# Optimization experiments

Measured on AMD Instinct MI355X. Metric: run time of the kernel, lower is better.

The kernel has to match this reference:

```python
import jax, jax.numpy as jnp
import numpy as np
from jax import lax

# SSD300/COCO geometry
B, P, C = 16, 8732, 81
V_CENTER, V_SIZE = 0.1, 0.2        # box coder variances
SCORE_THRESH = 0.05
NMS_THRESH = 0.45
DETS_PER_IMG = 100
PRE_NMS_TOPK = 1000                # fixed-size candidate set for jit-compatible NMS
MIN_SIZE = 0.01                    # remove_small_boxes threshold


def setup_inputs() -> dict:
    key = jax.random.key(0)
    k1, k2, k3, k4, k5 = jax.random.split(key, 5)
    # scale logits so a realistic fraction of softmax scores clears SCORE_THRESH
    pred_logits = jax.random.normal(k1, (B, P, C), jnp.float32) * 2.0
    pred_boxes = jax.random.normal(k2, (B, P, 4), jnp.float32) * 0.5
    # priors in (cx, cy, w, h), normalized coords, positive sizes
    cxcy = jax.random.uniform(k3, (P, 2), jnp.float32, 0.05, 0.95)
    wh = jax.random.uniform(k4, (P, 2), jnp.float32, 0.02, 0.4)
    priors = jnp.concatenate([cxcy, wh], axis=-1)
    target_sizes = jax.random.randint(k5, (B, 2), 480, 1333)  # (h, w) per image
    return {"pred_logits": pred_logits, "pred_boxes": pred_boxes,
            "priors": priors, "target_sizes": target_sizes}


def _decode(rel, priors):
    # SSD box coder: rel = (dx, dy, dw, dh), priors = (cx, cy, w, h) -> xyxy
    cxcy = priors[:, :2] + rel[:, :2] * V_CENTER * priors[:, 2:]
    wh = priors[:, 2:] * jnp.exp(rel[:, 2:] * V_SIZE)
    return jnp.concatenate([cxcy - 0.5 * wh, cxcy + 0.5 * wh], axis=-1)


def _pairwise_iou(b):
    # b: [K, 4] xyxy
    area = (b[:, 2] - b[:, 0]) * (b[:, 3] - b[:, 1])
    lt = jnp.maximum(b[:, None, :2], b[None, :, :2])
    rb = jnp.minimum(b[:, None, 2:], b[None, :, 2:])
    whi = jnp.clip(rb - lt, 0.0)
    inter = whi[..., 0] * whi[..., 1]
    return inter / (area[:, None] + area[None, :] - inter + 1e-9)


def _per_image(logits, rel, priors, size_hw):
    nc1 = C - 1  # foreground classes
    # decode and scale to pixel coords: target_size.flip(0).repeat(2) = [w, h, w, h]
    size_hw = size_hw.astype(jnp.float32)
    whwh = jnp.concatenate([size_hw[::-1], size_hw[::-1]])
    boxes = _decode(rel, priors) * whwh                     # [P, 4]
    scores = jax.nn.softmax(logits, axis=-1)[:, 1:]          # [P, C-1], drop background
    # score threshold + remove_small_boxes, fused as a mask (jit-safe)
    size_ok = ((boxes[:, 2] - boxes[:, 0]) >= MIN_SIZE) & \
              ((boxes[:, 3] - boxes[:, 1]) >= MIN_SIZE)      # [P]
    valid = (scores > SCORE_THRESH) & size_ok[:, None]       # [P, C-1]
    s_flat = jnp.where(valid, scores, -1.0).reshape(-1)      # [P*(C-1)]
    vals, idx = lax.top_k(s_flat, PRE_NMS_TOPK)
    prior_idx = idx // nc1
    labels_k = idx % nc1 + 1                                 # class ids in [1, C)
    boxes_k = boxes[prior_idx]                               # [K, 4]
    vmask = vals > 0.0                                       # real candidates
    # batched_nms via per-class coordinate offset
    max_coord = jnp.max(jnp.where(vmask[:, None], boxes_k, 0.0))
    offs_boxes = boxes_k + (labels_k.astype(jnp.float32) * (max_coord + 1.0))[:, None]
    iou = _pairwise_iou(offs_boxes)                          # [K, K]
    cols = jnp.arange(PRE_NMS_TOPK)

    def body(i, keep):
        suppress = (iou[i] > NMS_THRESH) & keep[i] & (cols > i)
        return keep & ~suppress

    keep = lax.fori_loop(0, PRE_NMS_TOPK, body, vmask)
    kept_scores = jnp.where(keep, vals, -1.0)
    fvals, fidx = lax.top_k(kept_scores, DETS_PER_IMG)
    fvalid = fvals > 0.0
    out_boxes = jnp.where(fvalid[:, None], boxes_k[fidx], 0.0)
    out_scores = jnp.where(fvalid, fvals, 0.0)
    out_labels = jnp.where(fvalid, labels_k[fidx], -1)
    return out_boxes, out_scores, out_labels


def reference(pred_logits, pred_boxes, priors, target_sizes):
    boxes, scores, labels = jax.vmap(_per_image, in_axes=(0, 0, None, 0))(
        pred_logits, pred_boxes, priors, target_sizes)
    # padded, fixed-size equivalent of the per-image list of dicts
    return boxes, scores, labels
```

## Files before the change

### kernel.cpp

```cpp
#include <hip/hip_runtime.h>
#include <math.h>

#pragma clang fp contract(off)

#define NIMG 16
#define NP   8732
#define NCLS 81
#define NFG  80
#define KTOP 1000
#define KPAD 1024
#define DETS 100
#define CAPMAX 166912
#define BASEBITS 0x3D000000u
#define CNT_STRIDE 64
#define TILEB 137
#define NB 640

#define OFF_BOXES  0u
#define OFF_CNT    2235392u
#define OFF_GHIST  2239488u
#define OFF_CSCORE 2280448u
#define OFF_CLABEL 2345984u
#define OFF_CBOX   2411520u
#define OFF_COFFS  2673664u
#define OFF_CAREA  2935808u
#define OFF_VALIDW 3001344u
#define OFF_MASK   3003392u
#define OFF_CAND   5100544u
#define MEMSET_LEN 45056u

typedef unsigned long long u64;
typedef unsigned int u32;

#define AS_GLOBAL __attribute__((address_space(1)))
#define AS_LOCAL  __attribute__((address_space(3)))

__global__ __launch_bounds__(256, 6) void k_decode(
    const float* __restrict__ logits, const float* __restrict__ rel,
    const float* __restrict__ priors, const int* __restrict__ tsz,
    float* __restrict__ boxes_out, u64* __restrict__ cand,
    u32* __restrict__ cnt, u32* __restrict__ ghist, int cap)
{
#pragma clang fp contract(off)
    __shared__ __align__(16) float lx[64 * NCLS];
    __shared__ float pmx[4 * 64];
    __shared__ float psm[4 * 64];
    __shared__ u32 sok[64];
    __shared__ u32 wtt[4];
    __shared__ u32 sbase;
    __shared__ u32 lhist[NB];
    int b  = blockIdx.x / TILEB;
    int g  = blockIdx.x - b * TILEB;
    int p0 = g * 64;
    int t  = threadIdx.x;
    int lane = t & 63;
    int q = t >> 6;
    int npri = NP - p0; if (npri > 64) npri = 64;
    int words = npri * NCLS;

    const u32* s32 = (const u32*)(logits + ((size_t)b * NP + p0) * NCLS);
    u32* lxw = (u32*)lx;
    int full = words >> 8;
    for (int k = q; k < full; k += 4)
        __builtin_amdgcn_global_load_lds(
            (AS_GLOBAL const u32*)(s32 + (k << 8) + (lane << 2)),
            (AS_LOCAL u32*)(lxw + (k << 8)), 16, 0, 0);
    int base = full << 8;
    int c4 = (words - base) >> 6;
    for (int k = q; k < c4; k += 4)
        __builtin_amdgcn_global_load_lds(
            (AS_GLOBAL const u32*)(s32 + base + (k << 6) + lane),
            (AS_LOCAL u32*)(lxw + base + (k << 6)), 4, 0, 0);
    int base2 = base + (c4 << 6);
    if (q == 0 && lane < words - base2) lxw[base2 + lane] = s32[base2 + lane];

    for (int i = t; i < NB; i += 256) lhist[i] = 0;

    int p = p0 + lane;
    bool active = p < NP;

    if (q == 0) {
        u32 ok = 0;
        if (active) {
            float4 pr = ((const float4*)priors)[p];
            float4 rl = ((const float4*)rel)[(size_t)b * NP + p];
            float W = (float)tsz[b * 2 + 1], H = (float)tsz[b * 2 + 0];
            float cx = pr.x + (rl.x * 0.1f) * pr.z;
            float cy = pr.y + (rl.y * 0.1f) * pr.w;
            float w_ = pr.z * expf(rl.z * 0.2f);
            float h_ = pr.w * expf(rl.w * 0.2f);
            float4 bx;
            bx.x = (cx - 0.5f * w_) * W; bx.y = (cy - 0.5f * h_) * H;
            bx.z = (cx + 0.5f * w_) * W; bx.w = (cy + 0.5f * h_) * H;
            ((float4*)boxes_out)[(size_t)b * NP + p] = bx;
            ok = ((bx.z - bx.x) >= 0.01f) && ((bx.w - bx.y) >= 0.01f);
        }
        sok[lane] = ok;
    }
    __syncthreads();

    int tb = lane * NCLS;
    int nk = (q == 0) ? 21 : 20;
    float x[21];
    #pragma unroll
    for (int k = 0; k < 21; ++k) {
        int c = q + 4 * k;
        x[k] = (k < nk) ? lx[tb + c] : -3.4e38f;
    }
    float pm = -3.4e38f;
    #pragma unroll
    for (int k = 0; k < 21; ++k) if (k < nk) pm = fmaxf(pm, x[k]);
    pmx[q * 64 + lane] = pm;
    __syncthreads();
    float m = fmaxf(fmaxf(pmx[lane], pmx[64 + lane]),
                    fmaxf(pmx[128 + lane], pmx[192 + lane]));

    float ps = 0.f;
    #pragma unroll
    for (int k = 0; k < 21; ++k) {
        if (k < nk) { x[k] = expf(x[k] - m); ps += x[k]; }
    }
    psm[q * 64 + lane] = ps;
    __syncthreads();
    float s = (psm[lane] + psm[64 + lane]) + (psm[128 + lane] + psm[192 + lane]);

    float hi = 0.05000075f * s;
    float lo = 0.04999925f * s;
    u32 pass = 0, band = 0;
    u32 sizeok = sok[lane];
    if (active && sizeok) {
        #pragma unroll
        for (int k = 0; k < 21; ++k) {
            int c = q + 4 * k;
            if (k < nk && c >= 1) {
                bool pa = x[k] > hi;
                bool bd = (!pa) && (x[k] > lo);
                pass |= ((u32)pa) << k;
                band |= ((u32)bd) << k;
            }
        }
    }
    while (band) {
        int k = __builtin_ctz(band); band &= band - 1;
        int c = q + 4 * k;
        float e = expf(lx[tb + c] - m);
        if (e / s > 0.05f) pass |= 1u << k;
    }
    int cnt_t = __popc(pass);

    int pre = cnt_t;
    #pragma unroll
    for (int d = 1; d < 64; d <<= 1) {
        int o = __shfl_up(pre, d);
        if (lane >= d) pre += o;
    }
    if (lane == 63) wtt[q] = (u32)pre;
    __syncthreads();
    u32 before = 0;
    for (int w = 0; w < 4; ++w) if (w < q) before += wtt[w];
    if (t == 0) {
        u32 tot = wtt[0] + wtt[1] + wtt[2] + wtt[3];
        sbase = tot ? atomicAdd(cnt + b * CNT_STRIDE, tot) : 0u;
    }
    __syncthreads();
    u32 pos = sbase + before + (u32)(pre - cnt_t);

    u64* cb = cand + (size_t)b * cap;
    u32 flatneg = 0xFFFFFFFFu - (u32)p * NFG;
    while (pass) {
        int k = __builtin_ctz(pass); pass &= pass - 1;
        int c = q + 4 * k;
        float e = expf(lx[tb + c] - m);
        float d = e / s;
        if ((int)pos < cap) {
            u32 sb = __float_as_uint(d);
            cb[pos] = ((u64)sb << 32) | (u64)(flatneg - (u32)(c - 1));
            u32 bin = (sb - BASEBITS) >> 16; if (bin > NB - 1) bin = NB - 1;
            atomicAdd(&lhist[bin], 1u);
        }
        ++pos;
    }
    __syncthreads();
    u32* gh = ghist + b * NB;
    for (int i = t; i < NB; i += 256) {
        u32 v = lhist[i];
        if (v) atomicAdd(gh + i, v);
    }
}

__device__ __forceinline__ void suffix_find(
    u32* hist, u32* wt, u32 K, int tid,
    volatile int* outI, volatile u32* outNext)
{
    int lane = tid & 63, w = tid >> 6;
    u32 v[8]; u32 tot = 0;
    #pragma unroll
    for (int k = 0; k < 8; ++k) { v[k] = hist[tid * 8 + k]; tot += v[k]; }
    u32 ws = tot;
    #pragma unroll
    for (int d = 1; d < 64; d <<= 1) {
        u32 o = __shfl_down(ws, d);
        if (lane + d < 64) ws += o;
    }
    if (lane == 0) wt[w] = ws;
    __syncthreads();
    u32 tail = 0;
    for (int w2 = w + 1; w2 < 16; ++w2) tail += wt[w2];
    u32 after = (ws - tot) + tail;
    u32 sufk[9];
    sufk[8] = after;
    #pragma unroll
    for (int k = 7; k >= 0; --k) sufk[k] = v[k] + sufk[k + 1];
    #pragma unroll
    for (int k = 0; k < 8; ++k) {
        if (sufk[k] >= K && sufk[k + 1] < K) {
            *outI = tid * 8 + k;
            *outNext = sufk[k + 1];
        }
    }
    __syncthreads();
}

__global__ __launch_bounds__(1024) void k_select(
    const u64* __restrict__ cand, const u32* __restrict__ cnt,
    const u32* __restrict__ ghist, const float* __restrict__ boxes,
    float* __restrict__ cscore, int* __restrict__ clabel,
    float4* __restrict__ cbox, float4* __restrict__ coffs,
    float* __restrict__ carea, u64* __restrict__ validw, int cap)
{
#pragma clang fp contract(off)
    __shared__ u32 h[NB];
    __shared__ u32 fh[8192];
    __shared__ u32 wt[16];
    __shared__ u64 buf[2048];
    __shared__ float red16[16];
    __shared__ int sh_c, sh_i2;
    __shared__ u32 sh_S, sh_next, sh_d, sh_m;
    int b = blockIdx.x, t = threadIdx.x, lane = t & 63;
    u32 n = min(cnt[b * CNT_STRIDE], (u32)cap);
    const u64* cb = cand + (size_t)b * cap;

    for (int i = t; i < NB; i += 1024) h[i] = ghist[b * NB + i];
    if (t == 0) { sh_c = -2; sh_i2 = -2; sh_S = 0; sh_next = 0; sh_m = 0; }
    __syncthreads();
    if (t < 64) {
        u32 v[10]; u32 tot = 0;
        #pragma unroll
        for (int k = 0; k < 10; ++k) { v[k] = h[t * 10 + k]; tot += v[k]; }
        u32 ws = tot;
        #pragma unroll
        for (int d = 1; d < 64; d <<= 1) {
            u32 o = (u32)__shfl_down((int)ws, d);
            if (t + d < 64) ws += o;
        }
        u32 suf[11];
        suf[10] = ws - tot;
        #pragma unroll
        for (int k = 9; k >= 0; --k) suf[k] = v[k] + suf[k + 1];
        #pragma unroll
        for (int k = 0; k < 10; ++k) {
            if (suf[k] >= (u32)KTOP && suf[k + 1] < (u32)KTOP) {
                sh_c = t * 10 + k; sh_S = suf[k]; sh_next = suf[k + 1];
            }
        }
    }
    __syncthreads();
    int c = sh_c;
    u32 T = 0;
    if (c >= 0) {
        u32 Tc = BASEBITS + ((u32)c << 16);
        if (sh_S <= 2048u) {
            T = Tc;
        } else {
            u32 nhi = sh_next;
            for (int i = t; i < 8192; i += 1024) fh[i] = 0;
            __syncthreads();
            for (u32 i = (u32)t; i < n; i += 1024) {
                u32 sb = (u32)(cb[i] >> 32);
                if ((sb & 0xFFFF0000u) == Tc)
                    atomicAdd(&fh[(sb >> 3) & 0x1FFFu], 1u);
            }
            __syncthreads();
            suffix_find(fh, wt, (u32)KTOP - nhi, t, &sh_i2, &sh_d);
            T = (sh_i2 >= 0) ? (Tc + ((u32)sh_i2 << 3)) : Tc;
        }
    }
    for (u32 bs0 = 0; bs0 < n; bs0 += 4096) {
        u32 i0 = bs0 + (u32)t;
        u64 k0 = 0, k1 = 0, k2 = 0, k3 = 0;
        bool q0 = i0 < n, q1 = i0 + 1024 < n, q2 = i0 + 2048 < n, q3 = i0 + 3072 < n;
        if (q0) k0 = cb[i0];
        if (q1) k1 = cb[i0 + 1024];
        if (q2) k2 = cb[i0 + 2048];
        if (q3) k3 = cb[i0 + 3072];
        #pragma unroll
        for (int e = 0; e < 4; ++e) {
            u64 key = (e == 0) ? k0 : (e == 1) ? k1 : (e == 2) ? k2 : k3;
            bool pr = (e == 0) ? q0 : (e == 1) ? q1 : (e == 2) ? q2 : q3;
            bool pick = pr && ((u32)(key >> 32) >= T);
            u64 bal = __ballot(pick);
            u32 wb = 0;
            if (lane == 0 && bal) wb = atomicAdd(&sh_m, (u32)__popcll(bal));
            wb = (u32)__shfl((int)wb, 0);
            if (pick) {
                u32 pos = wb + (u32)__popcll(bal & ((1ULL << lane) - 1ULL));
                if (pos < 2048) buf[pos] = key;
            }
        }
    }
    __syncthreads();
    u32 m = min(sh_m, 2048u);
    for (int i = t; i < 2048; i += 1024) if ((u32)i >= m) buf[i] = 0ULL;
    __syncthreads();
    for (int k = 2; k <= 2048; k <<= 1) {
        for (int j = k >> 1; j >= 64; j >>= 1) {
            #pragma unroll
            for (int e = 0; e < 2; ++e) {
                int i = t + e * 1024;
                int ixj = i ^ j;
                if (ixj > i) {
                    u64 a = buf[i], bb = buf[ixj];
                    bool up = (i & k) == 0;
                    if (up ? (a < bb) : (a > bb)) { buf[i] = bb; buf[ixj] = a; }
                }
            }
            __syncthreads();
        }
        u64 v0 = buf[t], v1 = buf[t + 1024];
        bool up0 = (t & k) == 0;
        bool up1 = ((t + 1024) & k) == 0;
        int js = ((k >> 1) < 32) ? (k >> 1) : 32;
        for (int j = js; j >= 1; j >>= 1) {
            u64 o0 = __shfl_xor(v0, j);
            u64 o1 = __shfl_xor(v1, j);
            bool lo0 = (t & j) == 0;
            v0 = (lo0 == up0) ? (v0 > o0 ? v0 : o0) : (v0 < o0 ? v0 : o0);
            v1 = (lo0 == up1) ? (v1 > o1 ? v1 : o1) : (v1 < o1 ? v1 : o1);
        }
        buf[t] = v0; buf[t + 1024] = v1;
        __syncthreads();
    }
    u64 key = (t < KTOP) ? buf[t] : 0ULL;
    float s = __uint_as_float((u32)(key >> 32));
    bool valid = s > 0.0f;
    u32 flat = valid ? (0xFFFFFFFFu - (u32)key) : 0u;
    int prior = (int)(flat / NFG);
    int cls = (int)(flat - (u32)prior * NFG) + 1;
    float4 bx = make_float4(0.f, 0.f, 0.f, 0.f);
    if (valid) bx = ((const float4*)boxes)[b * NP + prior];
    cscore[b * KPAD + t] = s;
    clabel[b * KPAD + t] = cls;
    cbox[b * KPAD + t] = bx;
    u64 vb = __ballot(valid);
    if (lane == 0) validw[b * 16 + (t >> 6)] = vb;
    float lm = valid ? fmaxf(fmaxf(bx.x, bx.y), fmaxf(bx.z, bx.w)) : 0.0f;
    lm = fmaxf(lm, 0.0f);
    #pragma unroll
    for (int d = 1; d < 64; d <<= 1) lm = fmaxf(lm, __shfl_xor(lm, d));
    if (lane == 0) red16[t >> 6] = lm;
    __syncthreads();
    float mc = red16[0];
    #pragma unroll
    for (int w = 1; w < 16; ++w) mc = fmaxf(mc, red16[w]);
    float off = (float)cls * (mc + 1.0f);
    float4 ob = valid ? make_float4(bx.x + off, bx.y + off, bx.z + off, bx.w + off)
                      : make_float4(0.f, 0.f, 0.f, 0.f);
    float area = valid ? (ob.z - ob.x) * (ob.w - ob.y) : 0.0f;
    coffs[b * KPAD + t] = ob;
    carea[b * KPAD + t] = area;
}

__global__ __launch_bounds__(1024) void k_iou(
    const float4* __restrict__ coffs, const float* __restrict__ carea,
    u64* __restrict__ cmask)
{
#pragma clang fp contract(off)
    __shared__ float4 bs[KPAD];
    __shared__ float as_[KPAD];
    int b = blockIdx.x >> 4, tile = blockIdx.x & 15;
    int t = threadIdx.x;
    bs[t] = coffs[b * KPAD + t];
    as_[t] = carea[b * KPAD + t];
    __syncthreads();
    int j = tile * 64 + (t & 63);
    int w = t >> 6;
    float4 bj = bs[j];
    float aj = as_[j];
    int r0 = w * 64;
    u64 bits = 0;
    #pragma unroll 4
    for (int k = 0; k < 64; ++k) {
        int r = r0 + k;
        float4 br = bs[r];
        float ar = as_[r];
        float ltx = fmaxf(br.x, bj.x), lty = fmaxf(br.y, bj.y);
        float rbx = fminf(br.z, bj.z), rby = fminf(br.w, bj.w);
        float wx = fmaxf(rbx - ltx, 0.0f), wy = fmaxf(rby - lty, 0.0f);
        float inter = wx * wy;
        float denom = ((ar + aj) - inter) + 1e-9f;
        float iou = inter / denom;
        bool sup = (iou > 0.45f) && (j > r);
        bits |= ((u64)sup) << k;
    }
    cmask[((size_t)b * 16 + w) * KPAD + j] = bits;
}

__global__ __launch_bounds__(64) void k_nms(
    const u64* __restrict__ cmask, const u64* __restrict__ validw,
    const float* __restrict__ cscore, const int* __restrict__ clabel,
    const float4* __restrict__ cbox, float* __restrict__ out)
{
    int b = blockIdx.x, lane = threadIdx.x;
    const u64* cm = cmask + (size_t)b * 16 * KPAD;
    u64 kept[16];
    u64 cw[16];
    #pragma unroll
    for (int w = 0; w < 16; ++w) cw[w] = cm[w * KPAD + lane];
    #pragma unroll
    for (int g = 0; g < 16; ++g) {
        u64 vg = validw[b * 16 + g];
        bool rem = false;
        #pragma unroll
        for (int w = 0; w < 16; ++w)
            if (w < g) rem |= (kept[w] & cw[w]) != 0ULL;
        u64 cg = cw[g];
        bool myv = ((vg >> lane) & 1ULL) && !rem;
        if (g < 15) {
            int cbase = (g + 1) * 64 + lane;
            #pragma unroll
            for (int w = 0; w < 16; ++w) cw[w] = cm[w * KPAD + cbase];
        }
        u64 K = __ballot(myv);
        for (;;) {
            u64 K2 = __ballot(myv && ((K & cg) == 0ULL));
            if (K2 == K) break;
            K = K2;
        }
        kept[g] = K;
    }
    __shared__ u64 sk[16];
    __shared__ int pfx[17];
    __shared__ int slot[DETS];
    if (lane == 0) {
        #pragma unroll
        for (int w = 0; w < 16; ++w) sk[w] = kept[w];
        int run = 0;
        #pragma unroll
        for (int l = 0; l < 16; ++l) { pfx[l] = run; run += __popcll(kept[l]); }
        pfx[16] = run;
    }
    __syncthreads();
    if (lane < 16) {
        int r = pfx[lane];
        u64 wv = sk[lane];
        while (wv && r < DETS) {
            int bit = __builtin_ctzll(wv);
            slot[r] = lane * 64 + bit;
            ++r;
            wv &= wv - 1;
        }
    }
    __syncthreads();
    int total = min(pfx[16], DETS);
    for (int r = lane; r < DETS; r += 64) {
        float4 bx = make_float4(0.f, 0.f, 0.f, 0.f);
        float s = 0.0f;
        int lb = -1;
        if (r < total) {
            int cdx = slot[r];
            bx = cbox[b * KPAD + cdx];
            s = cscore[b * KPAD + cdx];
            lb = clabel[b * KPAD + cdx];
        }
        float* ob = out + ((size_t)b * DETS + r) * 4;
        ob[0] = bx.x; ob[1] = bx.y; ob[2] = bx.z; ob[3] = bx.w;
        out[NIMG * DETS * 4 + b * DETS + r] = s;
        out[NIMG * DETS * 4 + NIMG * DETS + b * DETS + r] = (float)lb;
    }
}

extern "C" void kernel_launch(void* const* d_in, const int* in_sizes, int n_in,
                              void* d_out, int out_size, void* d_ws, size_t ws_size,
                              hipStream_t stream) {
    const float* logits = (const float*)d_in[0];
    const float* rel    = (const float*)d_in[1];
    const float* priors = (const float*)d_in[2];
    const int*   tsz    = (const int*)d_in[3];
    float* out = (float*)d_out;
    char* ws = (char*)d_ws;

    float* boxes  = (float*)(ws + OFF_BOXES);
    u32*   cnt    = (u32*)(ws + OFF_CNT);
    u32*   ghist  = (u32*)(ws + OFF_GHIST);
    float* cscore = (float*)(ws + OFF_CSCORE);
    int*   clabel = (int*)(ws + OFF_CLABEL);
    float4* cbox  = (float4*)(ws + OFF_CBOX);
    float4* coffs = (float4*)(ws + OFF_COFFS);
    float* carea  = (float*)(ws + OFF_CAREA);
    u64*   validw = (u64*)(ws + OFF_VALIDW);
    u64*   cmask  = (u64*)(ws + OFF_MASK);
    u64*   cand   = (u64*)(ws + OFF_CAND);

    long long avail = ((long long)ws_size - (long long)OFF_CAND) / (NIMG * 8);
    int cap = (int)(avail < CAPMAX ? (avail > 0 ? avail : 1) : CAPMAX);
    cap &= ~1;

    hipMemsetAsync(cnt, 0, MEMSET_LEN, stream);
    k_decode<<<NIMG * TILEB, 256, 0, stream>>>(logits, rel, priors, tsz,
                                               boxes, cand, cnt, ghist, cap);
    k_select<<<NIMG, 1024, 0, stream>>>(cand, cnt, ghist, boxes, cscore, clabel,
                                        cbox, coffs, carea, validw, cap);
    k_iou<<<NIMG * 16, 1024, 0, stream>>>(coffs, carea, cmask);
    k_nms<<<NIMG, 64, 0, stream>>>(cmask, validw, cscore, clabel, cbox, out);
}
```

Measured before the change: 156.4 us.

## Fuse IoU and NMS kernels via last-block atomic counter; widen select scan

The IoU mask kernel and the NMS kernel are merged into one launch. Each of the 16 tile blocks per image bumps an atomic counter, and the last block to finish loads the image's full suppression mask into shared memory and runs the greedy NMS and output writing. This removes one kernel launch and lets NMS read masks from LDS instead of global memory. It adds threadfence and atomic overhead plus a serial tail inside one block. Separately, the candidate gather loop in k_select now issues 8 loads per thread per iteration instead of 4, to raise memory-level parallelism.

```diff
diff --git a/kernel.cpp b/kernel.cpp
--- a/kernel.cpp
+++ b/kernel.cpp
@@ -285,26 +285,26 @@
             T = (sh_i2 >= 0) ? (Tc + ((u32)sh_i2 << 3)) : Tc;
         }
     }
-    for (u32 bs0 = 0; bs0 < n; bs0 += 4096) {
-        u32 i0 = bs0 + (u32)t;
-        u64 k0 = 0, k1 = 0, k2 = 0, k3 = 0;
-        bool q0 = i0 < n, q1 = i0 + 1024 < n, q2 = i0 + 2048 < n, q3 = i0 + 3072 < n;
-        if (q0) k0 = cb[i0];
-        if (q1) k1 = cb[i0 + 1024];
-        if (q2) k2 = cb[i0 + 2048];
-        if (q3) k3 = cb[i0 + 3072];
-        #pragma unroll
-        for (int e = 0; e < 4; ++e) {
-            u64 key = (e == 0) ? k0 : (e == 1) ? k1 : (e == 2) ? k2 : k3;
-            bool pr = (e == 0) ? q0 : (e == 1) ? q1 : (e == 2) ? q2 : q3;
-            bool pick = pr && ((u32)(key >> 32) >= T);
+    for (u32 bs0 = 0; bs0 < n; bs0 += 8192) {
+        u64 kk[8];
+        bool qq[8];
+        #pragma unroll
+        for (int e = 0; e < 8; ++e) {
+            u32 idx = bs0 + (u32)t + ((u32)e << 10);
+            qq[e] = idx < n;
+            kk[e] = 0ULL;
+            if (qq[e]) kk[e] = cb[idx];
+        }
+        #pragma unroll
+        for (int e = 0; e < 8; ++e) {
+            bool pick = qq[e] && ((u32)(kk[e] >> 32) >= T);
             u64 bal = __ballot(pick);
             u32 wb = 0;
             if (lane == 0 && bal) wb = atomicAdd(&sh_m, (u32)__popcll(bal));
             wb = (u32)__shfl((int)wb, 0);
             if (pick) {
                 u32 pos = wb + (u32)__popcll(bal & ((1ULL << lane) - 1ULL));
-                if (pos < 2048) buf[pos] = key;
+                if (pos < 2048) buf[pos] = kk[e];
             }
         }
     }
@@ -370,19 +370,28 @@
     carea[b * KPAD + t] = area;
 }
 
-__global__ __launch_bounds__(1024) void k_iou(
+__global__ __launch_bounds__(1024, 1) void k_iou_nms(
     const float4* __restrict__ coffs, const float* __restrict__ carea,
-    u64* __restrict__ cmask)
+    u64* __restrict__ cmask, u32* __restrict__ cnt,
+    const u64* __restrict__ validw, const float* __restrict__ cscore,
+    const int* __restrict__ clabel, const float4* __restrict__ cbox,
+    float* __restrict__ out)
 {
 #pragma clang fp contract(off)
-    __shared__ float4 bs[KPAD];
-    __shared__ float as_[KPAD];
+    __shared__ __align__(16) char smem[16 * KPAD * 8];
+    __shared__ u64 sk[16];
+    __shared__ int pfx[17];
+    __shared__ int slot[DETS];
+    __shared__ int sh_last;
+    float4* bs = (float4*)smem;
+    float* as_ = (float*)(smem + 16 * KPAD);
+    u64* smask = (u64*)smem;
     int b = blockIdx.x >> 4, tile = blockIdx.x & 15;
-    int t = threadIdx.x;
+    int t = threadIdx.x, lane = t & 63;
     bs[t] = coffs[b * KPAD + t];
     as_[t] = carea[b * KPAD + t];
     __syncthreads();
-    int j = tile * 64 + (t & 63);
+    int j = tile * 64 + lane;
     int w = t >> 6;
     float4 bj = bs[j];
     float aj = as_[j];
@@ -403,66 +412,68 @@
         bits |= ((u64)sup) << k;
     }
     cmask[((size_t)b * 16 + w) * KPAD + j] = bits;
-}
-
-__global__ __launch_bounds__(64) void k_nms(
-    const u64* __restrict__ cmask, const u64* __restrict__ validw,
-    const float* __restrict__ cscore, const int* __restrict__ clabel,
-    const float4* __restrict__ cbox, float* __restrict__ out)
-{
-    int b = blockIdx.x, lane = threadIdx.x;
-    const u64* cm = cmask + (size_t)b * 16 * KPAD;
-    u64 kept[16];
-    u64 cw[16];
-    #pragma unroll
-    for (int w = 0; w < 16; ++w) cw[w] = cm[w * KPAD + lane];
-    #pragma unroll
-    for (int g = 0; g < 16; ++g) {
-        u64 vg = validw[b * 16 + g];
-        bool rem = false;
-        #pragma unroll
-        for (int w = 0; w < 16; ++w)
-            if (w < g) rem |= (kept[w] & cw[w]) != 0ULL;
-        u64 cg = cw[g];
-        bool myv = ((vg >> lane) & 1ULL) && !rem;
-        if (g < 15) {
-            int cbase = (g + 1) * 64 + lane;
+
+    __syncthreads();
+    if (t == 0) {
+        __threadfence();
+        u32 old = atomicAdd(cnt + b * CNT_STRIDE + 1, 1u);
+        sh_last = (old == 15u);
+    }
+    __syncthreads();
+    if (!sh_last) return;
+    __threadfence();
+
+    {
+        const float4* cm4 = (const float4*)(cmask + (size_t)b * 16 * KPAD);
+        float4* sm4 = (float4*)smem;
+        for (int i = t; i < 8 * KPAD; i += 1024) sm4[i] = cm4[i];
+    }
+    __syncthreads();
+
+    if (t < 64) {
+        u64 kept[16];
+        #pragma unroll
+        for (int g = 0; g < 16; ++g) {
+            u64 vg = validw[b * 16 + g];
+            bool rem = false;
             #pragma unroll
-            for (int w = 0; w < 16; ++w) cw[w] = cm[w * KPAD + cbase];
-        }
-        u64 K = __ballot(myv);
-        for (;;) {
-            u64 K2 = __ballot(myv && ((K & cg) == 0ULL));
-            if (K2 == K) break;
-            K = K2;
-        }
-        kept[g] = K;
-    }
-    __shared__ u64 sk[16];
-    __shared__ int pfx[17];
-    __shared__ int slot[DETS];
-    if (lane == 0) {
-        #pragma unroll
-        for (int w = 0; w < 16; ++w) sk[w] = kept[w];
-        int run = 0;
-        #pragma unroll
-        for (int l = 0; l < 16; ++l) { pfx[l] = run; run += __popcll(kept[l]); }
-        pfx[16] = run;
-    }
-    __syncthreads();
-    if (lane < 16) {
-        int r = pfx[lane];
-        u64 wv = sk[lane];
+            for (int w2 = 0; w2 < 16; ++w2)
+                if (w2 < g)
+                    rem |= (kept[w2] & smask[w2 * KPAD + g * 64 + lane]) != 0ULL;
+            u64 cg = smask[g * KPAD + g * 64 + lane];
+            bool myv = ((vg >> lane) & 1ULL) && !rem;
+            u64 K = __ballot(myv);
+            for (;;) {
+                u64 K2 = __ballot(myv && ((K & cg) == 0ULL));
+                if (K2 == K) break;
+                K = K2;
+            }
+            kept[g] = K;
+        }
+        if (lane == 0) {
+            int run = 0;
+            #pragma unroll
+            for (int l = 0; l < 16; ++l) {
+                sk[l] = kept[l]; pfx[l] = run; run += __popcll(kept[l]);
+            }
+            pfx[16] = run;
+        }
+    }
+    __syncthreads();
+    if (t < 16) {
+        int r = pfx[t];
+        u64 wv = sk[t];
         while (wv && r < DETS) {
             int bit = __builtin_ctzll(wv);
-            slot[r] = lane * 64 + bit;
+            slot[r] = t * 64 + bit;
             ++r;
             wv &= wv - 1;
         }
     }
     __syncthreads();
     int total = min(pfx[16], DETS);
-    for (int r = lane; r < DETS; r += 64) {
+    if (t < DETS) {
+        int r = t;
         float4 bx = make_float4(0.f, 0.f, 0.f, 0.f);
         float s = 0.0f;
         int lb = -1;
@@ -510,6 +521,6 @@
                                                boxes, cand, cnt, ghist, cap);
     k_select<<<NIMG, 1024, 0, stream>>>(cand, cnt, ghist, boxes, cscore, clabel,
                                         cbox, coffs, carea, validw, cap);
-    k_iou<<<NIMG * 16, 1024, 0, stream>>>(coffs, carea, cmask);
-    k_nms<<<NIMG, 64, 0, stream>>>(cmask, validw, cscore, clabel, cbox, out);
+    k_iou_nms<<<NIMG * 16, 1024, 0, stream>>>(coffs, carea, cmask, cnt, validw,
+                                              cscore, clabel, cbox, out);
 }
```

Result: slower. 167.9 us (+7.3%).
